# Kernel optimization log

Hardware: AMD Instinct MI355X
Metric: run time of the kernel (lower is better)

## Reference

```python
import jax, jax.numpy as jnp
import numpy as np
from jax import lax

K = 8  # window / output_stride (hardcoded in original forward)
BN_EPS = 1e-5


def setup_inputs() -> dict:
    key = jax.random.key(0)
    ks = jax.random.split(key, 4)
    B, C, H, W = 4, 56, 320, 320
    return {
        "x": jax.random.normal(ks[0], (B, C, H, W), jnp.float32),
        "conv1_w": jax.random.normal(ks[1], (56, 56), jnp.float32) * 0.01,
        "conv1_b": jnp.zeros((56,), jnp.float32),
        "conv2_w": jax.random.normal(ks[2], (1, 56), jnp.float32) * 0.01,
        "conv2_b": jnp.zeros((1,), jnp.float32),
        "bn1_gamma": jnp.ones((56,), jnp.float32),
        "bn1_beta": jnp.zeros((56,), jnp.float32),
        "bn2_gamma": jnp.ones((1,), jnp.float32),
        "bn2_beta": jnp.zeros((1,), jnp.float32),
    }


def _batchnorm(y, gamma, beta):
    # training-mode BatchNorm2d: stats over (N, H, W) per channel
    mean = jnp.mean(y, axis=(0, 2, 3), keepdims=True)
    var = jnp.var(y, axis=(0, 2, 3), keepdims=True)
    yhat = (y - mean) * lax.rsqrt(var + BN_EPS)
    return yhat * gamma[None, :, None, None] + beta[None, :, None, None]


def _counter(x, w1, b1, w2, b2, g1, be1, g2, be2):
    # AvgPool2d(kernel=8, stride=1) -> [B,56,H-7,W-7]
    p = lax.reduce_window(x, 0.0, lax.add, (1, 1, K, K), (1, 1, 1, 1), "VALID") / (K * K)
    y = jnp.einsum("oc,bchw->bohw", w1, p) + b1[None, :, None, None]
    y = jax.nn.relu(_batchnorm(y, g1, be1))
    y = jnp.einsum("oc,bchw->bohw", w2, y) + b2[None, :, None, None]
    y = jax.nn.relu(_batchnorm(y, g2, be2))
    return y  # [B,1,Hc,Wc]


def _dynamic_unfolding(x, local_count):
    # x: [B,C,H,W], local_count: [B,1,H-7,W-7]
    B, C, H, W = x.shape
    Hc, Wc = H - K + 1, W - K + 1
    m = jnp.mean(x, axis=1)  # [B,H,W]
    # extract all 8x8 sliding windows -> [B,Hc,Wc,64]
    patches = jnp.stack(
        [m[:, di:di + Hc, dj:dj + Wc] for di in range(K) for dj in range(K)],
        axis=-1,
    )
    sm = jax.nn.softmax(patches, axis=-1)  # per-window softmax
    wgt = sm * local_count[:, 0, :, :, None]  # [B,Hc,Wc,64]
    # overlapping fold (scatter-add) back to [B,1,H,W]
    R = jnp.zeros((B, H, W), x.dtype)
    for di in range(K):
        for dj in range(K):
            R = R.at[:, di:di + Hc, dj:dj + Wc].add(wgt[..., di * K + dj])
    return R[:, None, :, :]


def reference(x, conv1_w, conv1_b, conv2_w, conv2_b, bn1_gamma, bn1_beta, bn2_gamma, bn2_beta):
    C_out = _counter(x, conv1_w, conv1_b, conv2_w, conv2_b, bn1_gamma, bn1_beta, bn2_gamma, bn2_beta)
    R = _dynamic_unfolding(x, C_out)
    return C_out, R
```

## Files before the change

kernel.cpp:

```cpp
#include <hip/hip_runtime.h>
#include <math.h>

#define B 4
#define C 56
#define H 320
#define W 320
#define HC 313
#define WC 313
#define NIMG (H*W)
#define NSP  (HC*WC)
#define NPIX (B*NSP)
#define NM   (B*NIMG)
#define BN_EPS 1e-5f
#define NGRID 512

#define PHR 39
#define NF4 390

typedef __attribute__((ext_vector_type(8))) short short8;
typedef __attribute__((ext_vector_type(16))) float float16;
typedef __attribute__((ext_vector_type(4))) float f32x4;
typedef __attribute__((ext_vector_type(4))) unsigned short u16x4;

__device__ __forceinline__ unsigned short f2bf(float v) {
  unsigned int u = __float_as_uint(v);
  return (unsigned short)((u + 0x7fffu + ((u >> 16) & 1u)) >> 16);
}

__global__ __launch_bounds__(256) void pool32_kernel(
    const float* __restrict__ x, float* __restrict__ Epart,
    unsigned short* __restrict__ p_t) {
  __shared__ float tin[PHR][40];
  __shared__ float hs[PHR][40];
  __shared__ unsigned short Pt[8][1024];
  const int tid = threadIdx.x;
  int bid = blockIdx.x;
  const int g = bid % 7; bid /= 7;
  const int b = bid & 3; bid >>= 2;
  const int ty = bid / 10, tx = bid - (bid / 10) * 10;
  const int i0 = ty * 32, j0 = tx * 32;
  const float* xg = x + ((size_t)b * C + g * 8) * NIMG;

  int r4[2], q4[2]; bool act[2], vld[2], inter[2]; size_t xoff[2];
  #pragma unroll
  for (int k = 0; k < 2; ++k) {
    int idx = tid + k * 256;
    r4[k] = idx / 10; q4[k] = idx - r4[k] * 10;
    act[k] = idx < NF4;
    vld[k] = act[k] && (i0 + r4[k] < H) && (j0 + q4[k] * 4 < W);
    inter[k] = act[k] && r4[k] < 32 && q4[k] < 8;
    xoff[k] = (size_t)(i0 + r4[k]) * W + j0 + q4[k] * 4;
  }
  f32x4 cur4[2], nxt4[2];
  #pragma unroll
  for (int k = 0; k < 2; ++k)
    cur4[k] = vld[k] ? *(const f32x4*)(xg + xoff[k]) : (f32x4){0.f, 0.f, 0.f, 0.f};

  f32x4 esum4[2] = {{0.f, 0.f, 0.f, 0.f}, {0.f, 0.f, 0.f, 0.f}};

  const int hr = tid >> 3, hg = (tid & 7) * 4;
  const int hr2 = (tid + 256) >> 3;
  const bool h2 = tid < (PHR * 8 - 256);
  const int vi = tid >> 3, vg = (tid & 7) * 4;

  #pragma unroll
  for (int c = 0; c < 8; ++c) {
    #pragma unroll
    for (int k = 0; k < 2; ++k) {
      if (act[k]) *(f32x4*)&tin[r4[k]][q4[k] * 4] = cur4[k];
      if (inter[k]) esum4[k] += cur4[k];
    }
    __syncthreads();
    if (c < 7) {
      const float* xp = xg + (size_t)(c + 1) * NIMG;
      #pragma unroll
      for (int k = 0; k < 2; ++k)
        nxt4[k] = vld[k] ? *(const f32x4*)(xp + xoff[k]) : (f32x4){0.f, 0.f, 0.f, 0.f};
    }
    {
      f32x4 a  = *(const f32x4*)&tin[hr][hg];
      f32x4 bv = *(const f32x4*)&tin[hr][hg + 4];
      f32x4 cv = *(const f32x4*)&tin[hr][hg + 8];
      float s0 = ((a[0] + a[1]) + (a[2] + a[3])) + ((bv[0] + bv[1]) + (bv[2] + bv[3]));
      float s1 = s0 - a[0] + cv[0];
      float s2 = s1 - a[1] + cv[1];
      float s3 = s2 - a[2] + cv[2];
      *(f32x4*)&hs[hr][hg] = (f32x4){s0, s1, s2, s3};
      if (h2) {
        f32x4 a2  = *(const f32x4*)&tin[hr2][hg];
        f32x4 b2  = *(const f32x4*)&tin[hr2][hg + 4];
        f32x4 c2  = *(const f32x4*)&tin[hr2][hg + 8];
        float t0 = ((a2[0] + a2[1]) + (a2[2] + a2[3])) + ((b2[0] + b2[1]) + (b2[2] + b2[3]));
        float t1 = t0 - a2[0] + c2[0];
        float t2 = t1 - a2[1] + c2[1];
        float t3 = t2 - a2[2] + c2[2];
        *(f32x4*)&hs[hr2][hg] = (f32x4){t0, t1, t2, t3};
      }
    }
    __syncthreads();
    {
      f32x4 s = *(const f32x4*)&hs[vi][vg];
      #pragma unroll
      for (int d = 1; d < 8; ++d) s += *(const f32x4*)&hs[vi + d][vg];
      u16x4 o;
      #pragma unroll
      for (int k = 0; k < 4; ++k) o[k] = f2bf(s[k] * (1.f / 64.f));
      *(u16x4*)&Pt[c][vi * 32 + vg] = o;
    }
    #pragma unroll
    for (int k = 0; k < 2; ++k) cur4[k] = nxt4[k];
  }
  __syncthreads();

  float* Eb = Epart + ((size_t)g * B + b) * NIMG;
  #pragma unroll
  for (int k = 0; k < 2; ++k)
    if (inter[k]) *(f32x4*)&Eb[(i0 + r4[k]) * W + j0 + q4[k] * 4] = esum4[k];

  unsigned short* pg = p_t + (size_t)g * NPIX * 8;
  #pragma unroll
  for (int k = 0; k < 4; ++k) {
    int idx = tid + k * 256;
    int i = idx >> 5, j = idx & 31;
    int gi = i0 + i, gj = j0 + j;
    if (gi < HC && gj < WC) {
      unsigned short t8[8];
      #pragma unroll
      for (int c2 = 0; c2 < 8; ++c2) t8[c2] = Pt[c2][idx];
      *(short8*)(pg + ((size_t)b * NSP + gi * WC + gj) * 8) = *(short8*)t8;
    }
  }
}

__global__ __launch_bounds__(256) void se_pool_kernel(
    const float* __restrict__ Epart, float* __restrict__ E, float* __restrict__ S) {
  __shared__ float tin[39][40];
  __shared__ float hs[39][33];
  const int b = blockIdx.z;
  const int i0 = blockIdx.y * 32, j0 = blockIdx.x * 32;
  const int tid = threadIdx.x;
  for (int idx = tid; idx < 39 * 39; idx += 256) {
    int r = idx / 39, cc = idx - r * 39;
    int gi = i0 + r, gj = j0 + cc;
    float v = 0.f;
    if (gi < H && gj < W) {
      float s = 0.f;
      #pragma unroll
      for (int g = 0; g < 7; ++g)
        s += Epart[((size_t)g * B + b) * NIMG + gi * W + gj];
      v = expf(s * (1.f / C));
      if (r < 32 && cc < 32) E[(size_t)b * NIMG + gi * W + gj] = v;
    }
    tin[r][cc] = v;
  }
  __syncthreads();
  for (int idx = tid; idx < 39 * 32; idx += 256) {
    int r = idx >> 5, j = idx & 31;
    float s = 0.f;
    #pragma unroll
    for (int d = 0; d < 8; ++d) s += tin[r][j + d];
    hs[r][j] = s;
  }
  __syncthreads();
  for (int idx = tid; idx < 32 * 32; idx += 256) {
    int i = idx >> 5, j = idx & 31;
    int gi = i0 + i, gj = j0 + j;
    if (gi < HC && gj < WC) {
      float s = 0.f;
      #pragma unroll
      for (int d = 0; d < 8; ++d) s += hs[i + d][j];
      S[(size_t)b * NSP + gi * WC + gj] = s;
    }
  }
}

__global__ __launch_bounds__(256) void y1_stats_kernel(
    const unsigned short* __restrict__ p_t, const float* __restrict__ w1,
    float* __restrict__ ypart) {
  __shared__ unsigned short Wl[64 * 64];
  __shared__ float red[4][32][64];
  const int tid = threadIdx.x, wave = tid >> 6, lane = tid & 63;
  for (int idx = tid; idx < 4096; idx += 256) {
    int o = idx >> 6, k = idx & 63;
    float v = (o < C && k < C) ? w1[o * C + k] : 0.f;
    *(unsigned short*)((char*)Wl + (o * 128 + ((2 * k) ^ ((o & 7) << 4)))) = f2bf(v);
  }
  __syncthreads();
  short8 afr[2][4];
  #pragma unroll
  for (int q = 0; q < 2; ++q)
    #pragma unroll
    for (int ks = 0; ks < 4; ++ks) {
      int row = q * 32 + (lane & 31), kb = ks * 16 + 8 * (lane >> 5);
      afr[q][ks] = *(const short8*)((const char*)Wl + row * 128 + ((2 * kb) ^ ((row & 7) << 4)));
    }
  float s1[2][16], s2[2][16];
  #pragma unroll
  for (int q = 0; q < 2; ++q)
    #pragma unroll
    for (int r = 0; r < 16; ++r) { s1[q][r] = 0.f; s2[q][r] = 0.f; }

  const int h = lane >> 5;
  const int nchunk = (NPIX + 127) / 128;
  auto loadch = [&](int cc, short8* dst) {
    int col = cc * 128 + wave * 32 + (lane & 31);
    bool cv = (cc < nchunk) && (col < NPIX);
    size_t pofs = (size_t)(cv ? col : 0) * 8;
    #pragma unroll
    for (int ks = 0; ks < 4; ++ks) {
      int gg = ks * 2 + h;
      short8 bv = (short8){0, 0, 0, 0, 0, 0, 0, 0};
      if (gg < 7 && cv) bv = *(const short8*)(p_t + (size_t)gg * NPIX * 8 + pofs);
      dst[ks] = bv;
    }
  };
  short8 bfr[4];
  loadch(blockIdx.x, bfr);
  for (int ch = blockIdx.x; ch < nchunk; ch += NGRID) {
    short8 nbfr[4];
    loadch(ch + NGRID, nbfr);
    float16 a0 = {}, a1 = {};
    #pragma unroll
    for (int ks = 0; ks < 4; ++ks) {
      a0 = __builtin_amdgcn_mfma_f32_32x32x16_bf16(afr[0][ks], bfr[ks], a0, 0, 0, 0);
      a1 = __builtin_amdgcn_mfma_f32_32x32x16_bf16(afr[1][ks], bfr[ks], a1, 0, 0, 0);
    }
    #pragma unroll
    for (int r = 0; r < 16; ++r) {
      s1[0][r] += a0[r]; s2[0][r] = fmaf(a0[r], a0[r], s2[0][r]);
      s1[1][r] += a1[r]; s2[1][r] = fmaf(a1[r], a1[r], s2[1][r]);
    }
    #pragma unroll
    for (int ks = 0; ks < 4; ++ks) bfr[ks] = nbfr[ks];
  }
  for (int pass = 0; pass < 2; ++pass) {
    __syncthreads();
    #pragma unroll
    for (int q = 0; q < 2; ++q)
      #pragma unroll
      for (int r = 0; r < 16; ++r)
        red[wave][q * 16 + r][lane] = pass ? s2[q][r] : s1[q][r];
    __syncthreads();
    if (tid < C) {
      int row = tid, q = row >> 5, rr = row & 31;
      int hh = (rr >> 2) & 1, reg = (rr & 3) | ((rr >> 3) << 2);
      float s = 0.f;
      #pragma unroll
      for (int w = 0; w < 4; ++w)
        #pragma unroll
        for (int cl = 0; cl < 32; ++cl)
          s += red[w][q * 16 + reg][32 * hh + cl];
      ypart[blockIdx.x * 112 + pass * 56 + row] = s;
    }
  }
}

__global__ void ypart_bn1_kernel(const float* __restrict__ ypart,
                                 const float* __restrict__ g1, const float* __restrict__ be1,
                                 float* __restrict__ ac) {
  __shared__ float sums[112];
  int t = threadIdx.x;
  if (t < 112) {
    float s0 = 0.f, s1 = 0.f, s2 = 0.f, s3 = 0.f;
    #pragma unroll 4
    for (int b = 0; b < NGRID; b += 4) {
      s0 += ypart[(b + 0) * 112 + t];
      s1 += ypart[(b + 1) * 112 + t];
      s2 += ypart[(b + 2) * 112 + t];
      s3 += ypart[(b + 3) * 112 + t];
    }
    sums[t] = (s0 + s1) + (s2 + s3);
  }
  __syncthreads();
  if (t < C) {
    float m = sums[t] * (1.f / NPIX);
    float var = sums[56 + t] * (1.f / NPIX) - m * m;
    float a = g1[t] * rsqrtf(var + BN_EPS);
    ac[t] = a;
    ac[C + t] = fmaf(-a, m, be1[t]);
  }
}

__global__ __launch_bounds__(256) void y2_kernel(
    const unsigned short* __restrict__ p_t, const float* __restrict__ w1,
    const float* __restrict__ ac, const float* __restrict__ w2,
    float* __restrict__ y2, float* __restrict__ y2part) {
  __shared__ unsigned short Wl[64 * 64];
  __shared__ float af[64], cf[64], wf[64];
  const int tid = threadIdx.x, wave = tid >> 6, lane = tid & 63;
  for (int idx = tid; idx < 4096; idx += 256) {
    int o = idx >> 6, k = idx & 63;
    float v = (o < C && k < C) ? w1[o * C + k] : 0.f;
    *(unsigned short*)((char*)Wl + (o * 128 + ((2 * k) ^ ((o & 7) << 4)))) = f2bf(v);
  }
  if (tid < 64) {
    bool ok = tid < C;
    af[tid] = ok ? ac[tid] : 0.f;
    cf[tid] = ok ? ac[C + tid] : 0.f;
    wf[tid] = ok ? w2[tid] : 0.f;
  }
  __syncthreads();
  short8 afr[2][4];
  #pragma unroll
  for (int q = 0; q < 2; ++q)
    #pragma unroll
    for (int ks = 0; ks < 4; ++ks) {
      int row = q * 32 + (lane & 31), kb = ks * 16 + 8 * (lane >> 5);
      afr[q][ks] = *(const short8*)((const char*)Wl + row * 128 + ((2 * kb) ^ ((row & 7) << 4)));
    }
  const int h = lane >> 5;
  float ss1 = 0.f, ss2 = 0.f;
  const int nchunk = (NPIX + 127) / 128;
  auto loadch = [&](int cc, short8* dst) {
    int col = cc * 128 + wave * 32 + (lane & 31);
    bool cv = (cc < nchunk) && (col < NPIX);
    size_t pofs = (size_t)(cv ? col : 0) * 8;
    #pragma unroll
    for (int ks = 0; ks < 4; ++ks) {
      int gg = ks * 2 + h;
      short8 bv = (short8){0, 0, 0, 0, 0, 0, 0, 0};
      if (gg < 7 && cv) bv = *(const short8*)(p_t + (size_t)gg * NPIX * 8 + pofs);
      dst[ks] = bv;
    }
  };
  short8 bfr[4];
  loadch(blockIdx.x, bfr);
  for (int ch = blockIdx.x; ch < nchunk; ch += NGRID) {
    short8 nbfr[4];
    loadch(ch + NGRID, nbfr);
    float16 a0 = {}, a1 = {};
    #pragma unroll
    for (int ks = 0; ks < 4; ++ks) {
      a0 = __builtin_amdgcn_mfma_f32_32x32x16_bf16(afr[0][ks], bfr[ks], a0, 0, 0, 0);
      a1 = __builtin_amdgcn_mfma_f32_32x32x16_bf16(afr[1][ks], bfr[ks], a1, 0, 0, 0);
    }
    float ysum = 0.f;
    #pragma unroll
    for (int r = 0; r < 16; ++r) {
      int o0 = (r & 3) + 8 * (r >> 2) + 4 * h;
      ysum = fmaf(wf[o0], fmaxf(fmaf(af[o0], a0[r], cf[o0]), 0.f), ysum);
      int o1 = o0 + 32;
      ysum = fmaf(wf[o1], fmaxf(fmaf(af[o1], a1[r], cf[o1]), 0.f), ysum);
    }
    ysum += __shfl_xor(ysum, 32);
    int col = ch * 128 + wave * 32 + (lane & 31);
    bool wr = (col < NPIX) && lane < 32;
    if (wr) {
      y2[col] = ysum;
      ss1 += ysum;
      ss2 = fmaf(ysum, ysum, ss2);
    }
    #pragma unroll
    for (int ks = 0; ks < 4; ++ks) bfr[ks] = nbfr[ks];
  }
  #pragma unroll
  for (int off = 1; off < 64; off <<= 1) {
    ss1 += __shfl_xor(ss1, off);
    ss2 += __shfl_xor(ss2, off);
  }
  if (lane == 0) {
    y2part[(blockIdx.x * 4 + wave) * 2 + 0] = ss1;
    y2part[(blockIdx.x * 4 + wave) * 2 + 1] = ss2;
  }
}

__global__ void bn2_final_kernel(const float* __restrict__ y2part,
                                 const float* __restrict__ g2, const float* __restrict__ be2,
                                 float* __restrict__ a2c2) {
  __shared__ float red[8];
  int t = threadIdx.x;
  float s1 = 0.f, s2 = 0.f;
  for (int i = t; i < NGRID * 4; i += 256) {
    s1 += y2part[i * 2 + 0];
    s2 += y2part[i * 2 + 1];
  }
  #pragma unroll
  for (int off = 32; off > 0; off >>= 1) {
    s1 += __shfl_down(s1, off);
    s2 += __shfl_down(s2, off);
  }
  int wave = t >> 6, lane = t & 63;
  if (lane == 0) { red[wave * 2] = s1; red[wave * 2 + 1] = s2; }
  __syncthreads();
  if (t == 0) {
    s1 = red[0] + red[2] + red[4] + red[6];
    s2 = red[1] + red[3] + red[5] + red[7];
    float mean = s1 * (1.f / NPIX);
    float var  = s2 * (1.f / NPIX) - mean * mean;
    float a = g2[0] * rsqrtf(var + BN_EPS);
    a2c2[0] = a;
    a2c2[1] = fmaf(-a, mean, be2[0]);
  }
}

__global__ __launch_bounds__(256) void r_pool_kernel(
    const float* __restrict__ y2, const float* __restrict__ S,
    const float* __restrict__ a2c2, const float* __restrict__ E,
    float* __restrict__ cout, float* __restrict__ R) {
  __shared__ float tin[39][40];
  __shared__ float hs[39][33];
  const int b = blockIdx.z;
  const int i0 = blockIdx.y * 32, j0 = blockIdx.x * 32;
  const int tid = threadIdx.x;
  const float a2 = a2c2[0], c2 = a2c2[1];
  const float* y2b = y2 + (size_t)b * NSP;
  const float* Sb  = S + (size_t)b * NSP;
  float* cb = cout + (size_t)b * NSP;
  for (int idx = tid; idx < 39 * 39; idx += 256) {
    int r = idx / 39, cc = idx - r * 39;
    int gi = i0 + r - 7, gj = j0 + cc - 7;
    float t = 0.f;
    if (gi >= 0 && gi < HC && gj >= 0 && gj < WC) {
      float v = fmaxf(fmaf(a2, y2b[gi * WC + gj], c2), 0.f);
      t = v / Sb[gi * WC + gj];
      if (r >= 7 && cc >= 7) cb[gi * WC + gj] = v;
    }
    tin[r][cc] = t;
  }
  __syncthreads();
  for (int idx = tid; idx < 39 * 32; idx += 256) {
    int r = idx >> 5, j = idx & 31;
    float s = 0.f;
    #pragma unroll
    for (int d = 0; d < 8; ++d) s += tin[r][j + d];
    hs[r][j] = s;
  }
  __syncthreads();
  for (int idx = tid; idx < 32 * 32; idx += 256) {
    int i = idx >> 5, j = idx & 31;
    size_t gofs = (size_t)b * NIMG + (i0 + i) * W + (j0 + j);
    float s = 0.f;
    #pragma unroll
    for (int d = 0; d < 8; ++d) s += hs[i + d][j];
    R[gofs] = E[gofs] * s;
  }
}

extern "C" void kernel_launch(void* const* d_in, const int* in_sizes, int n_in,
                              void* d_out, int out_size, void* d_ws, size_t ws_size,
                              hipStream_t stream) {
  const float* x   = (const float*)d_in[0];
  const float* w1  = (const float*)d_in[1];
  const float* w2  = (const float*)d_in[3];
  const float* g1  = (const float*)d_in[5];
  const float* be1 = (const float*)d_in[6];
  const float* g2  = (const float*)d_in[7];
  const float* be2 = (const float*)d_in[8];

  float* out_c = (float*)d_out;
  float* out_r = out_c + NPIX;

  unsigned short* p_t = (unsigned short*)d_ws;
  float* fbase = (float*)(p_t + (size_t)7 * NPIX * 8);
  size_t off = 0;
  float* Epart  = fbase + off; off += (size_t)7 * NM;
  float* E      = fbase + off; off += NM;
  float* Sarr   = fbase + off; off += NPIX;
  float* y2     = fbase + off; off += NPIX;
  float* ypart  = fbase + off; off += (size_t)NGRID * 112;
  float* y2part = fbase + off; off += (size_t)NGRID * 8;
  float* ac     = fbase + off; off += 112;
  float* a2c2   = fbase + off; off += 2;

  pool32_kernel<<<100 * B * 7, 256, 0, stream>>>(x, Epart, p_t);

  dim3 sg(10, 10, B);
  se_pool_kernel<<<sg, 256, 0, stream>>>(Epart, E, Sarr);

  y1_stats_kernel<<<NGRID, 256, 0, stream>>>(p_t, w1, ypart);
  ypart_bn1_kernel<<<1, 128, 0, stream>>>(ypart, g1, be1, ac);
  y2_kernel<<<NGRID, 256, 0, stream>>>(p_t, w1, ac, w2, y2, y2part);
  bn2_final_kernel<<<1, 256, 0, stream>>>(y2part, g2, be2, a2c2);

  dim3 rg(10, 10, B);
  r_pool_kernel<<<rg, 256, 0, stream>>>(y2, Sarr, a2c2, E, out_c, out_r);
}
```

Measured before the change: 104.8 us.

## Fold BN2 finalize into r_pool, deepen channel prefetch, simplify box-filter passes

Removes the single-block bn2_final kernel launch by having every r_pool block redundantly reduce the y2 partial sums into shared memory before use. In pool32, loads are prefetched two channels ahead instead of one, and the vectorized sliding-sum horizontal and vertical passes become simple scalar 8-tap loops per output element. Fewer launches and serialized tiny kernels trade against redundant reduction work per block, more registers for prefetch, and more LDS reads in the scalar box filter.

```diff
diff --git a/kernel.cpp b/kernel.cpp
--- a/kernel.cpp
+++ b/kernel.cpp
@@ -20,7 +20,6 @@
 typedef __attribute__((ext_vector_type(8))) short short8;
 typedef __attribute__((ext_vector_type(16))) float float16;
 typedef __attribute__((ext_vector_type(4))) float f32x4;
-typedef __attribute__((ext_vector_type(4))) unsigned short u16x4;
 
 __device__ __forceinline__ unsigned short f2bf(float v) {
   unsigned int u = __float_as_uint(v);
@@ -31,7 +30,7 @@
     const float* __restrict__ x, float* __restrict__ Epart,
     unsigned short* __restrict__ p_t) {
   __shared__ float tin[PHR][40];
-  __shared__ float hs[PHR][40];
+  __shared__ float hs[PHR][32];
   __shared__ unsigned short Pt[8][1024];
   const int tid = threadIdx.x;
   int bid = blockIdx.x;
@@ -51,17 +50,14 @@
     inter[k] = act[k] && r4[k] < 32 && q4[k] < 8;
     xoff[k] = (size_t)(i0 + r4[k]) * W + j0 + q4[k] * 4;
   }
-  f32x4 cur4[2], nxt4[2];
-  #pragma unroll
-  for (int k = 0; k < 2; ++k)
+  f32x4 cur4[2], nx1[2], nx2[2];
+  #pragma unroll
+  for (int k = 0; k < 2; ++k) {
     cur4[k] = vld[k] ? *(const f32x4*)(xg + xoff[k]) : (f32x4){0.f, 0.f, 0.f, 0.f};
+    nx1[k]  = vld[k] ? *(const f32x4*)(xg + NIMG + xoff[k]) : (f32x4){0.f, 0.f, 0.f, 0.f};
+  }
 
   f32x4 esum4[2] = {{0.f, 0.f, 0.f, 0.f}, {0.f, 0.f, 0.f, 0.f}};
-
-  const int hr = tid >> 3, hg = (tid & 7) * 4;
-  const int hr2 = (tid + 256) >> 3;
-  const bool h2 = tid < (PHR * 8 - 256);
-  const int vi = tid >> 3, vg = (tid & 7) * 4;
 
   #pragma unroll
   for (int c = 0; c < 8; ++c) {
@@ -71,44 +67,35 @@
       if (inter[k]) esum4[k] += cur4[k];
     }
     __syncthreads();
-    if (c < 7) {
-      const float* xp = xg + (size_t)(c + 1) * NIMG;
+    if (c < 6) {
+      const float* xp = xg + (size_t)(c + 2) * NIMG;
       #pragma unroll
       for (int k = 0; k < 2; ++k)
-        nxt4[k] = vld[k] ? *(const f32x4*)(xp + xoff[k]) : (f32x4){0.f, 0.f, 0.f, 0.f};
-    }
-    {
-      f32x4 a  = *(const f32x4*)&tin[hr][hg];
-      f32x4 bv = *(const f32x4*)&tin[hr][hg + 4];
-      f32x4 cv = *(const f32x4*)&tin[hr][hg + 8];
-      float s0 = ((a[0] + a[1]) + (a[2] + a[3])) + ((bv[0] + bv[1]) + (bv[2] + bv[3]));
-      float s1 = s0 - a[0] + cv[0];
-      float s2 = s1 - a[1] + cv[1];
-      float s3 = s2 - a[2] + cv[2];
-      *(f32x4*)&hs[hr][hg] = (f32x4){s0, s1, s2, s3};
-      if (h2) {
-        f32x4 a2  = *(const f32x4*)&tin[hr2][hg];
-        f32x4 b2  = *(const f32x4*)&tin[hr2][hg + 4];
-        f32x4 c2  = *(const f32x4*)&tin[hr2][hg + 8];
-        float t0 = ((a2[0] + a2[1]) + (a2[2] + a2[3])) + ((b2[0] + b2[1]) + (b2[2] + b2[3]));
-        float t1 = t0 - a2[0] + c2[0];
-        float t2 = t1 - a2[1] + c2[1];
-        float t3 = t2 - a2[2] + c2[2];
-        *(f32x4*)&hs[hr2][hg] = (f32x4){t0, t1, t2, t3};
+        nx2[k] = vld[k] ? *(const f32x4*)(xp + xoff[k]) : (f32x4){0.f, 0.f, 0.f, 0.f};
+    }
+    #pragma unroll
+    for (int it = 0; it < 5; ++it) {
+      int idx = tid + it * 256;
+      if (idx < PHR * 32) {
+        int r = idx >> 5, j = idx & 31;
+        float s = 0.f;
+        #pragma unroll
+        for (int d = 0; d < 8; ++d) s += tin[r][j + d];
+        hs[r][j] = s;
       }
     }
     __syncthreads();
-    {
-      f32x4 s = *(const f32x4*)&hs[vi][vg];
-      #pragma unroll
-      for (int d = 1; d < 8; ++d) s += *(const f32x4*)&hs[vi + d][vg];
-      u16x4 o;
-      #pragma unroll
-      for (int k = 0; k < 4; ++k) o[k] = f2bf(s[k] * (1.f / 64.f));
-      *(u16x4*)&Pt[c][vi * 32 + vg] = o;
-    }
-    #pragma unroll
-    for (int k = 0; k < 2; ++k) cur4[k] = nxt4[k];
+    #pragma unroll
+    for (int it = 0; it < 4; ++it) {
+      int idx = tid + it * 256;
+      int i = idx >> 5, j = idx & 31;
+      float s = 0.f;
+      #pragma unroll
+      for (int d = 0; d < 8; ++d) s += hs[i + d][j];
+      Pt[c][idx] = f2bf(s * (1.f / 64.f));
+    }
+    #pragma unroll
+    for (int k = 0; k < 2; ++k) { cur4[k] = nx1[k]; nx1[k] = nx2[k]; }
   }
   __syncthreads();
 
@@ -364,45 +351,45 @@
   }
 }
 
-__global__ void bn2_final_kernel(const float* __restrict__ y2part,
-                                 const float* __restrict__ g2, const float* __restrict__ be2,
-                                 float* __restrict__ a2c2) {
-  __shared__ float red[8];
-  int t = threadIdx.x;
-  float s1 = 0.f, s2 = 0.f;
-  for (int i = t; i < NGRID * 4; i += 256) {
-    s1 += y2part[i * 2 + 0];
-    s2 += y2part[i * 2 + 1];
-  }
-  #pragma unroll
-  for (int off = 32; off > 0; off >>= 1) {
-    s1 += __shfl_down(s1, off);
-    s2 += __shfl_down(s2, off);
-  }
-  int wave = t >> 6, lane = t & 63;
-  if (lane == 0) { red[wave * 2] = s1; red[wave * 2 + 1] = s2; }
-  __syncthreads();
-  if (t == 0) {
-    s1 = red[0] + red[2] + red[4] + red[6];
-    s2 = red[1] + red[3] + red[5] + red[7];
-    float mean = s1 * (1.f / NPIX);
-    float var  = s2 * (1.f / NPIX) - mean * mean;
-    float a = g2[0] * rsqrtf(var + BN_EPS);
-    a2c2[0] = a;
-    a2c2[1] = fmaf(-a, mean, be2[0]);
-  }
-}
-
 __global__ __launch_bounds__(256) void r_pool_kernel(
     const float* __restrict__ y2, const float* __restrict__ S,
-    const float* __restrict__ a2c2, const float* __restrict__ E,
+    const float* __restrict__ y2part,
+    const float* __restrict__ g2, const float* __restrict__ be2,
+    const float* __restrict__ E,
     float* __restrict__ cout, float* __restrict__ R) {
   __shared__ float tin[39][40];
   __shared__ float hs[39][33];
+  __shared__ float bnred[8];
+  __shared__ float a2c2s[2];
   const int b = blockIdx.z;
   const int i0 = blockIdx.y * 32, j0 = blockIdx.x * 32;
   const int tid = threadIdx.x;
-  const float a2 = a2c2[0], c2 = a2c2[1];
+  {
+    float s1 = 0.f, s2 = 0.f;
+    for (int i = tid; i < NGRID * 4; i += 256) {
+      s1 += y2part[i * 2 + 0];
+      s2 += y2part[i * 2 + 1];
+    }
+    #pragma unroll
+    for (int off = 32; off > 0; off >>= 1) {
+      s1 += __shfl_down(s1, off);
+      s2 += __shfl_down(s2, off);
+    }
+    int wave = tid >> 6, lane = tid & 63;
+    if (lane == 0) { bnred[wave * 2] = s1; bnred[wave * 2 + 1] = s2; }
+    __syncthreads();
+    if (tid == 0) {
+      s1 = bnred[0] + bnred[2] + bnred[4] + bnred[6];
+      s2 = bnred[1] + bnred[3] + bnred[5] + bnred[7];
+      float mean = s1 * (1.f / NPIX);
+      float var  = s2 * (1.f / NPIX) - mean * mean;
+      float a = g2[0] * rsqrtf(var + BN_EPS);
+      a2c2s[0] = a;
+      a2c2s[1] = fmaf(-a, mean, be2[0]);
+    }
+    __syncthreads();
+  }
+  const float a2 = a2c2s[0], c2 = a2c2s[1];
   const float* y2b = y2 + (size_t)b * NSP;
   const float* Sb  = S + (size_t)b * NSP;
   float* cb = cout + (size_t)b * NSP;
@@ -460,7 +447,6 @@
   float* ypart  = fbase + off; off += (size_t)NGRID * 112;
   float* y2part = fbase + off; off += (size_t)NGRID * 8;
   float* ac     = fbase + off; off += 112;
-  float* a2c2   = fbase + off; off += 2;
 
   pool32_kernel<<<100 * B * 7, 256, 0, stream>>>(x, Epart, p_t);
 
@@ -470,8 +456,7 @@
   y1_stats_kernel<<<NGRID, 256, 0, stream>>>(p_t, w1, ypart);
   ypart_bn1_kernel<<<1, 128, 0, stream>>>(ypart, g1, be1, ac);
   y2_kernel<<<NGRID, 256, 0, stream>>>(p_t, w1, ac, w2, y2, y2part);
-  bn2_final_kernel<<<1, 256, 0, stream>>>(y2part, g2, be2, a2c2);
 
   dim3 rg(10, 10, B);
-  r_pool_kernel<<<rg, 256, 0, stream>>>(y2, Sarr, a2c2, E, out_c, out_r);
-}
+  r_pool_kernel<<<rg, 256, 0, stream>>>(y2, Sarr, y2part, g2, be2, E, out_c, out_r);
+}
```

After: 107.7 us. 1.03x slower.
